# Optimization experiments

Hardware: AMD Instinct MI355X
Metric: run time of the kernel (lower is better)

## Reference

```python
import jax, jax.numpy as jnp
import numpy as np

B, S, H, E, I = 2, 1024, 1024, 8, 512
EPS = 1e-8  # torch F.cosine_similarity eps


def setup_inputs() -> dict:
    key = jax.random.key(0)
    ks = jax.random.split(key, 5)
    return {
        "hidden_states": jax.random.normal(ks[0], (B, S, H), dtype=jnp.float32),
        "expert_embeddings": jax.random.normal(ks[1], (E, H), dtype=jnp.float32),
        # torch init is zeros; -0.03 keeps the zero-selection fallback (which NaNs the
        # original's softmax) from ever triggering while preserving ~half-dense routing
        "gate_threshold": jnp.full((E,), -0.03, dtype=jnp.float32),
        "w_gate": jax.random.normal(ks[2], (E, H, I), dtype=jnp.float32) / np.sqrt(H).astype(np.float32),
        "w_up": jax.random.normal(ks[3], (E, H, I), dtype=jnp.float32) / np.sqrt(H).astype(np.float32),
        "w_down": jax.random.normal(ks[4], (E, I, H), dtype=jnp.float32) / np.sqrt(I).astype(np.float32),
    }


def _forward(hidden_states, expert_embeddings, gate_threshold, w_gate, w_up, w_down):
    b, s, h = hidden_states.shape
    n_experts = expert_embeddings.shape[0]
    x = hidden_states.reshape(-1, h)  # [T, H]

    # cosine-similarity routing scores [T, E]
    xn = x / jnp.maximum(jnp.linalg.norm(x, axis=-1, keepdims=True), EPS)
    en = expert_embeddings / jnp.maximum(jnp.linalg.norm(expert_embeddings, axis=-1, keepdims=True), EPS)
    scores = xn @ en.T

    # SiLUHardThreshold forward: hard 0/1 mask (used only as a boolean downstream,
    # so no gradient flows through it in the module's output path)
    routing_mask = (jax.nn.silu(scores - gate_threshold) > 0).astype(scores.dtype)

    # guarantee at least one expert per token: fall back to top-1 score
    num_sel = routing_mask.sum(axis=-1)  # [T]
    top1 = jnp.argmax(scores, axis=-1)   # [T]
    routing_mask_final = jnp.where((num_sel == 0)[:, None],
                                   jax.nn.one_hot(top1, n_experts, dtype=scores.dtype),
                                   routing_mask)

    # softmax over selected experts (pre-fallback mask, as in the original)
    masked_scores = jnp.where(routing_mask > 0, scores, -jnp.inf)
    routing_weights = jax.nn.softmax(masked_scores.astype(jnp.float32), axis=-1).astype(x.dtype)
    gates = routing_weights * routing_mask_final  # [T, E] combine weights

    # per-expert Qwen3 SwiGLU MLP: down(silu(gate(x)) * up(x)); dense over experts,
    # gated combine is the vectorized equivalent of the gather/MLP/index_add loop
    hmid = jax.nn.silu(jnp.einsum('th,ehi->eti', x, w_gate)) * jnp.einsum('th,ehi->eti', x, w_up)  # [E,T,I]
    out = jnp.einsum('eti,eih,te->th', hmid, w_down, gates)  # [T, H]

    return out.reshape(b, s, h), scores


def reference(hidden_states, expert_embeddings, gate_threshold, w_gate, w_up, w_down):
    # returns (final_hidden_states [B,S,H], router_logits [T,E])
    return _forward(hidden_states, expert_embeddings, gate_threshold, w_gate, w_up, w_down)
```

## Files before the change

### kernel.cpp

```cpp
#include <hip/hip_runtime.h>
#include <hip/hip_bf16.h>
#include <stdint.h>

#define T_TOK 2048
#define H_DIM 1024
#define E_NUM 8
#define I_DIM 512
#define KDOWN (E_NUM * I_DIM)
#define EPSR 1e-8f

typedef short s16x8 __attribute__((ext_vector_type(8)));
typedef float f32x4 __attribute__((ext_vector_type(4)));

static __device__ __forceinline__ uint16_t f2bf(float f) {
    union { float f; uint32_t i; } v; v.f = f;
    uint32_t lsb = (v.i >> 16) & 1u;
    v.i += 0x7fffu + lsb;
    return (uint16_t)(v.i >> 16);
}

static __device__ __forceinline__ void gll16(const void* g, void* l) {
    __builtin_amdgcn_global_load_lds(
        (const __attribute__((address_space(1))) void*)g,
        (__attribute__((address_space(3))) void*)l, 16, 0, 0);
}

__global__ __launch_bounds__(256) void cast_x_kernel(const float* __restrict__ x,
                                                     uint16_t* __restrict__ xb) {
    int i = (blockIdx.x * 256 + threadIdx.x) * 4;
    float4 v = *(const float4*)(x + i);
    ushort4 o;
    o.x = f2bf(v.x); o.y = f2bf(v.y); o.z = f2bf(v.z); o.w = f2bf(v.w);
    *(ushort4*)(xb + i) = o;
}

__global__ __launch_bounds__(256) void transpose_cast_kernel(
    const float* __restrict__ in, uint16_t* __restrict__ out,
    int C, long in_batch, long out_batch, int out_stride) {
    __shared__ float tile[64][68];
    const float* src = in + (long)blockIdx.z * in_batch;
    uint16_t* dst = out + (long)blockIdx.z * out_batch;
    const int r0 = blockIdx.y * 64, c0 = blockIdx.x * 64;
    const int tid = threadIdx.x;
    const int g16 = tid >> 4, l16 = (tid & 15) * 4;
    #pragma unroll
    for (int it = 0; it < 4; ++it) {
        int r = it * 16 + g16;
        *(float4*)&tile[r][l16] = *(const float4*)(src + (long)(r0 + r) * C + c0 + l16);
    }
    __syncthreads();
    #pragma unroll
    for (int it = 0; it < 4; ++it) {
        int oc = it * 16 + g16;
        ushort4 o;
        o.x = f2bf(tile[l16 + 0][oc]);
        o.y = f2bf(tile[l16 + 1][oc]);
        o.z = f2bf(tile[l16 + 2][oc]);
        o.w = f2bf(tile[l16 + 3][oc]);
        *(ushort4*)(dst + (long)(c0 + oc) * out_stride + r0 + l16) = o;
    }
}

__global__ __launch_bounds__(256) void routing_kernel(
    const float* __restrict__ x, const float* __restrict__ emb,
    const float* __restrict__ thr, float* __restrict__ scores_out,
    float* __restrict__ gates) {
    __shared__ float semb[E_NUM * H_DIM];
    __shared__ float senorm[E_NUM];
    const int tid = threadIdx.x;
    const int lane = tid & 63;
    const int wave = tid >> 6;
    for (int i = tid; i < E_NUM * H_DIM; i += 256) semb[i] = emb[i];
    __syncthreads();
    for (int e = wave; e < E_NUM; e += 4) {
        float s = 0.f;
        #pragma unroll
        for (int c = 0; c < 16; ++c) { float v = semb[e * H_DIM + lane + 64 * c]; s += v * v; }
        #pragma unroll
        for (int off = 32; off; off >>= 1) s += __shfl_xor(s, off);
        if (lane == 0) senorm[e] = fmaxf(sqrtf(s), EPSR);
    }
    __syncthreads();
    const int t = blockIdx.x * 4 + wave;
    const float* xt = x + (long)t * H_DIM;
    float nrm = 0.f, dot[E_NUM];
    #pragma unroll
    for (int e = 0; e < E_NUM; ++e) dot[e] = 0.f;
    #pragma unroll
    for (int c = 0; c < 16; ++c) {
        float v = xt[lane + 64 * c];
        nrm += v * v;
        #pragma unroll
        for (int e = 0; e < E_NUM; ++e) dot[e] += v * semb[e * H_DIM + lane + 64 * c];
    }
    #pragma unroll
    for (int off = 32; off; off >>= 1) {
        nrm += __shfl_xor(nrm, off);
        #pragma unroll
        for (int e = 0; e < E_NUM; ++e) dot[e] += __shfl_xor(dot[e], off);
    }
    float xn = fmaxf(sqrtf(nrm), EPSR);
    float sc[E_NUM], sel[E_NUM];
    float msel = -1e30f, mall = -1e30f;
    int nsel = 0, arg = 0;
    #pragma unroll
    for (int e = 0; e < E_NUM; ++e) {
        sc[e] = dot[e] / (xn * senorm[e]);
        float d = sc[e] - thr[e];
        sel[e] = (d > 0.f) ? 1.f : 0.f;
        if (d > 0.f) { nsel++; msel = fmaxf(msel, sc[e]); }
        if (sc[e] > mall) { mall = sc[e]; arg = e; }
    }
    float w[E_NUM], den = 0.f;
    #pragma unroll
    for (int e = 0; e < E_NUM; ++e) { w[e] = (sel[e] > 0.f) ? __expf(sc[e] - msel) : 0.f; den += w[e]; }
    if (lane == 0) {
        #pragma unroll
        for (int e = 0; e < E_NUM; ++e) {
            scores_out[t * E_NUM + e] = sc[e];
            gates[t * E_NUM + e] = (nsel > 0) ? (w[e] / den) : ((e == arg) ? 1.f : 0.f);
        }
    }
}

__global__ __launch_bounds__(256, 4) void moe_gateup_kernel(
    const uint16_t* __restrict__ xb,
    const uint16_t* __restrict__ wgT,
    const uint16_t* __restrict__ wuT,
    const float* __restrict__ gates,
    uint16_t* __restrict__ hmid) {
    const int e  = blockIdx.z;
    const int t0 = blockIdx.x * 128;
    const int i0 = blockIdx.y * 64;
    __shared__ uint16_t sA[128][64];
    __shared__ uint16_t sG[64][64];
    __shared__ uint16_t sU[64][64];
    __shared__ float sGate[128];
    const int tid  = threadIdx.x;
    const int lane = tid & 63;
    const int wave = tid >> 6;
    const int wm = wave >> 1, wn = wave & 1;
    if (tid < 128) sGate[tid] = gates[(t0 + tid) * E_NUM + e];

    const int srowA = wave * 32 + (lane >> 3);
    const int scA   = ((lane & 7) ^ (srowA & 7)) * 8;
    const int srowG = wave * 16 + (lane >> 3);
    const int scG   = ((lane & 7) ^ (srowG & 7)) * 8;
    const uint16_t* ga = xb  + (long)(t0 + srowA) * H_DIM + scA;
    const uint16_t* gg = wgT + ((long)e * I_DIM + i0 + srowG) * H_DIM + scG;
    const uint16_t* gu = wuT + ((long)e * I_DIM + i0 + srowG) * H_DIM + scG;

    f32x4 accg[4][2] = {};
    f32x4 accu[4][2] = {};
    const int q = lane >> 4, r16 = lane & 15;
    const int sw = r16 & 7;

    for (int kb = 0; kb < H_DIM; kb += 64) {
        __syncthreads();
        #pragma unroll
        for (int j = 0; j < 4; ++j)
            gll16(ga + (long)j * 8 * H_DIM + kb, &sA[wave * 32 + j * 8][0]);
        #pragma unroll
        for (int j = 0; j < 2; ++j) {
            gll16(gg + (long)j * 8 * H_DIM + kb, &sG[wave * 16 + j * 8][0]);
            gll16(gu + (long)j * 8 * H_DIM + kb, &sU[wave * 16 + j * 8][0]);
        }
        __syncthreads();
        #pragma unroll
        for (int kk = 0; kk < 2; ++kk) {
            s16x8 af[4], gf[2], uf[2];
            const int pc = ((kk * 4 + q) ^ sw) * 8;
            #pragma unroll
            for (int m = 0; m < 4; ++m)
                af[m] = *(const s16x8*)&sA[wm * 64 + m * 16 + r16][pc];
            #pragma unroll
            for (int n = 0; n < 2; ++n) {
                gf[n] = *(const s16x8*)&sG[wn * 32 + n * 16 + r16][pc];
                uf[n] = *(const s16x8*)&sU[wn * 32 + n * 16 + r16][pc];
            }
            #pragma unroll
            for (int m = 0; m < 4; ++m)
                #pragma unroll
                for (int n = 0; n < 2; ++n) {
                    accg[m][n] = __builtin_amdgcn_mfma_f32_16x16x32_bf16(af[m], gf[n], accg[m][n], 0, 0, 0);
                    accu[m][n] = __builtin_amdgcn_mfma_f32_16x16x32_bf16(af[m], uf[n], accu[m][n], 0, 0, 0);
                }
        }
    }
    #pragma unroll
    for (int m = 0; m < 4; ++m) {
        #pragma unroll
        for (int rr = 0; rr < 4; ++rr) {
            int trow = wm * 64 + m * 16 + q * 4 + rr;
            float gate = sGate[trow];
            long base = (long)(t0 + trow) * KDOWN + e * I_DIM + i0;
            #pragma unroll
            for (int n = 0; n < 2; ++n) {
                float g = accg[m][n][rr], u = accu[m][n][rr];
                float h = gate * (g / (1.f + __expf(-g))) * u;
                hmid[base + wn * 32 + n * 16 + r16] = f2bf(h);
            }
        }
    }
}

__global__ __launch_bounds__(256, 4) void moe_down_kernel(
    const uint16_t* __restrict__ hmid,
    const uint16_t* __restrict__ wdT,
    float* __restrict__ out,
    float* __restrict__ parts) {
    const int t0 = blockIdx.x * 128;
    const int h0 = blockIdx.y * 64;
    const int kz = blockIdx.z;
    const int kst  = kz ? kz * 1344 + 64 : 0;
    const int kend = (kz + 1) * 1344 + 64;
    __shared__ uint16_t sA[128][64];
    __shared__ uint16_t sB[64][64];
    const int tid  = threadIdx.x;
    const int lane = tid & 63;
    const int wave = tid >> 6;
    const int wm = wave >> 1, wn = wave & 1;

    const int srowA = wave * 32 + (lane >> 3);
    const int scA   = ((lane & 7) ^ (srowA & 7)) * 8;
    const int srowB = wave * 16 + (lane >> 3);
    const int scB   = ((lane & 7) ^ (srowB & 7)) * 8;
    const uint16_t* ga = hmid + (long)(t0 + srowA) * KDOWN + scA;
    const uint16_t* gb = wdT  + (long)(h0 + srowB) * KDOWN + scB;

    f32x4 acc[4][2] = {};
    const int q = lane >> 4, r16 = lane & 15;
    const int sw = r16 & 7;

    for (int kb = kst; kb < kend; kb += 64) {
        __syncthreads();
        #pragma unroll
        for (int j = 0; j < 4; ++j)
            gll16(ga + (long)j * 8 * KDOWN + kb, &sA[wave * 32 + j * 8][0]);
        #pragma unroll
        for (int j = 0; j < 2; ++j)
            gll16(gb + (long)j * 8 * KDOWN + kb, &sB[wave * 16 + j * 8][0]);
        __syncthreads();
        #pragma unroll
        for (int kk = 0; kk < 2; ++kk) {
            s16x8 af[4], bf[2];
            const int pc = ((kk * 4 + q) ^ sw) * 8;
            #pragma unroll
            for (int m = 0; m < 4; ++m)
                af[m] = *(const s16x8*)&sA[wm * 64 + m * 16 + r16][pc];
            #pragma unroll
            for (int n = 0; n < 2; ++n)
                bf[n] = *(const s16x8*)&sB[wn * 32 + n * 16 + r16][pc];
            #pragma unroll
            for (int m = 0; m < 4; ++m)
                #pragma unroll
                for (int n = 0; n < 2; ++n)
                    acc[m][n] = __builtin_amdgcn_mfma_f32_16x16x32_bf16(af[m], bf[n], acc[m][n], 0, 0, 0);
        }
    }
    float* dst = (kz == 0) ? out : (parts + (long)(kz - 1) * T_TOK * H_DIM);
    #pragma unroll
    for (int m = 0; m < 4; ++m) {
        #pragma unroll
        for (int rr = 0; rr < 4; ++rr) {
            int t = t0 + wm * 64 + m * 16 + q * 4 + rr;
            #pragma unroll
            for (int n = 0; n < 2; ++n)
                dst[(long)t * H_DIM + h0 + wn * 32 + n * 16 + r16] = acc[m][n][rr];
        }
    }
}

__global__ __launch_bounds__(256) void reduce_kernel(float* __restrict__ out,
                                                     const float* __restrict__ parts) {
    long i = ((long)blockIdx.x * 256 + threadIdx.x) * 4;
    float4 a = *(const float4*)(out + i);
    float4 b = *(const float4*)(parts + i);
    float4 c = *(const float4*)(parts + (long)T_TOK * H_DIM + i);
    a.x += b.x + c.x; a.y += b.y + c.y; a.z += b.z + c.z; a.w += b.w + c.w;
    *(float4*)(out + i) = a;
}

extern "C" void kernel_launch(void* const* d_in, const int* in_sizes, int n_in,
                              void* d_out, int out_size, void* d_ws, size_t ws_size,
                              hipStream_t stream) {
    const float* x    = (const float*)d_in[0];
    const float* emb  = (const float*)d_in[1];
    const float* thr  = (const float*)d_in[2];
    const float* wg   = (const float*)d_in[3];
    const float* wu   = (const float*)d_in[4];
    const float* wd   = (const float*)d_in[5];
    float* out    = (float*)d_out;
    float* scores = out + (size_t)T_TOK * H_DIM;

    uint8_t* ws = (uint8_t*)d_ws;
    uint16_t* xb   = (uint16_t*)(ws);
    uint16_t* wgT  = (uint16_t*)(ws + (size_t)4  * 1048576);
    uint16_t* wuT  = (uint16_t*)(ws + (size_t)12 * 1048576);
    uint16_t* wdT  = (uint16_t*)(ws + (size_t)20 * 1048576);
    uint16_t* hmid = (uint16_t*)(ws + (size_t)28 * 1048576);
    float*    gates = (float*)  (ws + (size_t)44 * 1048576);
    float*    parts = (float*)ws;

    cast_x_kernel<<<(T_TOK * H_DIM) / 1024, 256, 0, stream>>>(x, xb);
    transpose_cast_kernel<<<dim3(I_DIM / 64, H_DIM / 64, E_NUM), 256, 0, stream>>>(
        wg, wgT, I_DIM, (long)H_DIM * I_DIM, (long)I_DIM * H_DIM, H_DIM);
    transpose_cast_kernel<<<dim3(I_DIM / 64, H_DIM / 64, E_NUM), 256, 0, stream>>>(
        wu, wuT, I_DIM, (long)H_DIM * I_DIM, (long)I_DIM * H_DIM, H_DIM);
    transpose_cast_kernel<<<dim3(H_DIM / 64, I_DIM / 64, E_NUM), 256, 0, stream>>>(
        wd, wdT, H_DIM, (long)I_DIM * H_DIM, (long)I_DIM, KDOWN);
    routing_kernel<<<T_TOK / 4, 256, 0, stream>>>(x, emb, thr, scores, gates);
    moe_gateup_kernel<<<dim3(T_TOK / 128, I_DIM / 64, E_NUM), 256, 0, stream>>>(
        xb, wgT, wuT, gates, hmid);
    moe_down_kernel<<<dim3(T_TOK / 128, H_DIM / 64, 3), 256, 0, stream>>>(hmid, wdT, out, parts);
    reduce_kernel<<<(T_TOK * H_DIM) / 1024, 256, 0, stream>>>(out, parts);
}
```

Measured before the change: 190.0 us.

## Fuse prep kernels, double-buffer weights, load activations directly to registers

Merges the three weight transpose-casts into one launch and folds the x-to-bf16 cast into the routing kernel, cutting launches and one pass over x. The gate/up and down GEMMs switch to 256-token tiles where each wave owns 64 full rows and reads its A fragments straight from global memory into registers. Only the weight tiles stay in LDS, now double-buffered so the next tile prefetches during MFMAs. The down GEMM's split-K grows from 3 to 6 slices, with a 5-way partial reduction and the partials buffer moved to its own workspace region. Per-wave accumulator count doubles, which raises register pressure and lowers occupancy, and the uncoalesced direct global A loads are a risk.

```diff
diff --git a/kernel.cpp b/kernel.cpp
--- a/kernel.cpp
+++ b/kernel.cpp
@@ -25,22 +25,26 @@
         (__attribute__((address_space(3))) void*)l, 16, 0, 0);
 }
 
-__global__ __launch_bounds__(256) void cast_x_kernel(const float* __restrict__ x,
-                                                     uint16_t* __restrict__ xb) {
-    int i = (blockIdx.x * 256 + threadIdx.x) * 4;
-    float4 v = *(const float4*)(x + i);
-    ushort4 o;
-    o.x = f2bf(v.x); o.y = f2bf(v.y); o.z = f2bf(v.z); o.w = f2bf(v.w);
-    *(ushort4*)(xb + i) = o;
-}
-
-__global__ __launch_bounds__(256) void transpose_cast_kernel(
-    const float* __restrict__ in, uint16_t* __restrict__ out,
-    int C, long in_batch, long out_batch, int out_stride) {
+__global__ __launch_bounds__(256) void transpose_all_kernel(
+    const float* __restrict__ wg, const float* __restrict__ wu,
+    const float* __restrict__ wd, uint16_t* __restrict__ wgT,
+    uint16_t* __restrict__ wuT, uint16_t* __restrict__ wdT) {
     __shared__ float tile[64][68];
-    const float* src = in + (long)blockIdx.z * in_batch;
-    uint16_t* dst = out + (long)blockIdx.z * out_batch;
-    const int r0 = blockIdx.y * 64, c0 = blockIdx.x * 64;
+    const int z = blockIdx.z;
+    const float* src; uint16_t* dst; int C, out_stride, r0, c0;
+    if (z < 16) {
+        const int e = z & 7;
+        src = (z < 8 ? wg : wu) + (long)e * H_DIM * I_DIM;
+        dst = (z < 8 ? wgT : wuT) + (long)e * I_DIM * H_DIM;
+        C = I_DIM; out_stride = H_DIM;
+        r0 = blockIdx.y * 64; c0 = blockIdx.x * 64;
+    } else {
+        const int e = z - 16;
+        src = wd + (long)e * I_DIM * H_DIM;
+        dst = wdT + (long)e * I_DIM;
+        C = H_DIM; out_stride = KDOWN;
+        r0 = blockIdx.x * 64; c0 = blockIdx.y * 64;
+    }
     const int tid = threadIdx.x;
     const int g16 = tid >> 4, l16 = (tid & 15) * 4;
     #pragma unroll
@@ -64,7 +68,7 @@
 __global__ __launch_bounds__(256) void routing_kernel(
     const float* __restrict__ x, const float* __restrict__ emb,
     const float* __restrict__ thr, float* __restrict__ scores_out,
-    float* __restrict__ gates) {
+    float* __restrict__ gates, uint16_t* __restrict__ xb) {
     __shared__ float semb[E_NUM * H_DIM];
     __shared__ float senorm[E_NUM];
     const int tid = threadIdx.x;
@@ -83,12 +87,14 @@
     __syncthreads();
     const int t = blockIdx.x * 4 + wave;
     const float* xt = x + (long)t * H_DIM;
+    uint16_t* xbt = xb + (long)t * H_DIM;
     float nrm = 0.f, dot[E_NUM];
     #pragma unroll
     for (int e = 0; e < E_NUM; ++e) dot[e] = 0.f;
     #pragma unroll
     for (int c = 0; c < 16; ++c) {
         float v = xt[lane + 64 * c];
+        xbt[lane + 64 * c] = f2bf(v);
         nrm += v * v;
         #pragma unroll
         for (int e = 0; e < E_NUM; ++e) dot[e] += v * semb[e * H_DIM + lane + 64 * c];
@@ -123,150 +129,161 @@
     }
 }
 
-__global__ __launch_bounds__(256, 4) void moe_gateup_kernel(
+__global__ __launch_bounds__(256, 2) void moe_gateup_kernel(
     const uint16_t* __restrict__ xb,
     const uint16_t* __restrict__ wgT,
     const uint16_t* __restrict__ wuT,
     const float* __restrict__ gates,
     uint16_t* __restrict__ hmid) {
     const int e  = blockIdx.z;
-    const int t0 = blockIdx.x * 128;
+    const int t0 = blockIdx.x * 256;
     const int i0 = blockIdx.y * 64;
-    __shared__ uint16_t sA[128][64];
-    __shared__ uint16_t sG[64][64];
-    __shared__ uint16_t sU[64][64];
-    __shared__ float sGate[128];
+    __shared__ uint16_t sG[2][64][64];
+    __shared__ uint16_t sU[2][64][64];
+    __shared__ float sGate[256];
     const int tid  = threadIdx.x;
     const int lane = tid & 63;
     const int wave = tid >> 6;
-    const int wm = wave >> 1, wn = wave & 1;
-    if (tid < 128) sGate[tid] = gates[(t0 + tid) * E_NUM + e];
-
-    const int srowA = wave * 32 + (lane >> 3);
-    const int scA   = ((lane & 7) ^ (srowA & 7)) * 8;
-    const int srowG = wave * 16 + (lane >> 3);
-    const int scG   = ((lane & 7) ^ (srowG & 7)) * 8;
-    const uint16_t* ga = xb  + (long)(t0 + srowA) * H_DIM + scA;
-    const uint16_t* gg = wgT + ((long)e * I_DIM + i0 + srowG) * H_DIM + scG;
-    const uint16_t* gu = wuT + ((long)e * I_DIM + i0 + srowG) * H_DIM + scG;
-
-    f32x4 accg[4][2] = {};
-    f32x4 accu[4][2] = {};
+    sGate[tid] = gates[(t0 + tid) * E_NUM + e];
+
+    const int srow = wave * 16 + (lane >> 3);
+    const int scol = ((lane & 7) ^ (srow & 7)) * 8;
+    const uint16_t* gg = wgT + ((long)e * I_DIM + i0 + srow) * H_DIM + scol;
+    const uint16_t* gu = wuT + ((long)e * I_DIM + i0 + srow) * H_DIM + scol;
+
     const int q = lane >> 4, r16 = lane & 15;
     const int sw = r16 & 7;
-
-    for (int kb = 0; kb < H_DIM; kb += 64) {
-        __syncthreads();
-        #pragma unroll
-        for (int j = 0; j < 4; ++j)
-            gll16(ga + (long)j * 8 * H_DIM + kb, &sA[wave * 32 + j * 8][0]);
-        #pragma unroll
-        for (int j = 0; j < 2; ++j) {
-            gll16(gg + (long)j * 8 * H_DIM + kb, &sG[wave * 16 + j * 8][0]);
-            gll16(gu + (long)j * 8 * H_DIM + kb, &sU[wave * 16 + j * 8][0]);
-        }
-        __syncthreads();
+    const uint16_t* ax = xb + (long)(t0 + wave * 64 + r16) * H_DIM + q * 8;
+
+    f32x4 accg[4][4] = {}, accu[4][4] = {};
+
+    #pragma unroll
+    for (int j = 0; j < 2; ++j) {
+        gll16(gg + (long)j * 8 * H_DIM, &sG[0][wave * 16 + j * 8][0]);
+        gll16(gu + (long)j * 8 * H_DIM, &sU[0][wave * 16 + j * 8][0]);
+    }
+    __syncthreads();
+
+    for (int it = 0; it < 16; ++it) {
+        const int kb = it * 64;
+        const int b = it & 1;
+        s16x8 af[2][4];
+        #pragma unroll
+        for (int kk = 0; kk < 2; ++kk)
+            #pragma unroll
+            for (int m = 0; m < 4; ++m)
+                af[kk][m] = *(const s16x8*)(ax + (long)m * 16 * H_DIM + kb + kk * 32);
+        if (it < 15) {
+            #pragma unroll
+            for (int j = 0; j < 2; ++j) {
+                gll16(gg + (long)j * 8 * H_DIM + kb + 64, &sG[b ^ 1][wave * 16 + j * 8][0]);
+                gll16(gu + (long)j * 8 * H_DIM + kb + 64, &sU[b ^ 1][wave * 16 + j * 8][0]);
+            }
+        }
         #pragma unroll
         for (int kk = 0; kk < 2; ++kk) {
-            s16x8 af[4], gf[2], uf[2];
             const int pc = ((kk * 4 + q) ^ sw) * 8;
-            #pragma unroll
-            for (int m = 0; m < 4; ++m)
-                af[m] = *(const s16x8*)&sA[wm * 64 + m * 16 + r16][pc];
-            #pragma unroll
-            for (int n = 0; n < 2; ++n) {
-                gf[n] = *(const s16x8*)&sG[wn * 32 + n * 16 + r16][pc];
-                uf[n] = *(const s16x8*)&sU[wn * 32 + n * 16 + r16][pc];
+            s16x8 gf[4], uf[4];
+            #pragma unroll
+            for (int n = 0; n < 4; ++n) {
+                gf[n] = *(const s16x8*)&sG[b][n * 16 + r16][pc];
+                uf[n] = *(const s16x8*)&sU[b][n * 16 + r16][pc];
             }
             #pragma unroll
             for (int m = 0; m < 4; ++m)
                 #pragma unroll
-                for (int n = 0; n < 2; ++n) {
-                    accg[m][n] = __builtin_amdgcn_mfma_f32_16x16x32_bf16(af[m], gf[n], accg[m][n], 0, 0, 0);
-                    accu[m][n] = __builtin_amdgcn_mfma_f32_16x16x32_bf16(af[m], uf[n], accu[m][n], 0, 0, 0);
+                for (int n = 0; n < 4; ++n) {
+                    accg[m][n] = __builtin_amdgcn_mfma_f32_16x16x32_bf16(af[kk][m], gf[n], accg[m][n], 0, 0, 0);
+                    accu[m][n] = __builtin_amdgcn_mfma_f32_16x16x32_bf16(af[kk][m], uf[n], accu[m][n], 0, 0, 0);
                 }
         }
+        __syncthreads();
     }
     #pragma unroll
     for (int m = 0; m < 4; ++m) {
         #pragma unroll
         for (int rr = 0; rr < 4; ++rr) {
-            int trow = wm * 64 + m * 16 + q * 4 + rr;
-            float gate = sGate[trow];
-            long base = (long)(t0 + trow) * KDOWN + e * I_DIM + i0;
-            #pragma unroll
-            for (int n = 0; n < 2; ++n) {
+            const int trow = wave * 64 + m * 16 + q * 4 + rr;
+            const float gate = sGate[trow];
+            const long base = (long)(t0 + trow) * KDOWN + e * I_DIM + i0;
+            #pragma unroll
+            for (int n = 0; n < 4; ++n) {
                 float g = accg[m][n][rr], u = accu[m][n][rr];
                 float h = gate * (g / (1.f + __expf(-g))) * u;
-                hmid[base + wn * 32 + n * 16 + r16] = f2bf(h);
+                hmid[base + n * 16 + r16] = f2bf(h);
             }
         }
     }
 }
 
-__global__ __launch_bounds__(256, 4) void moe_down_kernel(
+__global__ __launch_bounds__(256, 3) void moe_down_kernel(
     const uint16_t* __restrict__ hmid,
     const uint16_t* __restrict__ wdT,
     float* __restrict__ out,
     float* __restrict__ parts) {
-    const int t0 = blockIdx.x * 128;
+    const int t0 = blockIdx.x * 256;
     const int h0 = blockIdx.y * 64;
     const int kz = blockIdx.z;
-    const int kst  = kz ? kz * 1344 + 64 : 0;
-    const int kend = (kz + 1) * 1344 + 64;
-    __shared__ uint16_t sA[128][64];
-    __shared__ uint16_t sB[64][64];
+    const int it0 = (kz < 4) ? kz * 11 : 44 + (kz - 4) * 10;
+    const int nit = (kz < 4) ? 11 : 10;
+    __shared__ uint16_t sB[2][64][64];
     const int tid  = threadIdx.x;
     const int lane = tid & 63;
     const int wave = tid >> 6;
-    const int wm = wave >> 1, wn = wave & 1;
-
-    const int srowA = wave * 32 + (lane >> 3);
-    const int scA   = ((lane & 7) ^ (srowA & 7)) * 8;
-    const int srowB = wave * 16 + (lane >> 3);
-    const int scB   = ((lane & 7) ^ (srowB & 7)) * 8;
-    const uint16_t* ga = hmid + (long)(t0 + srowA) * KDOWN + scA;
-    const uint16_t* gb = wdT  + (long)(h0 + srowB) * KDOWN + scB;
-
-    f32x4 acc[4][2] = {};
+
+    const int srow = wave * 16 + (lane >> 3);
+    const int scol = ((lane & 7) ^ (srow & 7)) * 8;
+    const uint16_t* gb = wdT + ((long)h0 + srow) * KDOWN + scol;
+
     const int q = lane >> 4, r16 = lane & 15;
     const int sw = r16 & 7;
-
-    for (int kb = kst; kb < kend; kb += 64) {
-        __syncthreads();
-        #pragma unroll
-        for (int j = 0; j < 4; ++j)
-            gll16(ga + (long)j * 8 * KDOWN + kb, &sA[wave * 32 + j * 8][0]);
-        #pragma unroll
-        for (int j = 0; j < 2; ++j)
-            gll16(gb + (long)j * 8 * KDOWN + kb, &sB[wave * 16 + j * 8][0]);
-        __syncthreads();
+    const uint16_t* ax = hmid + (long)(t0 + wave * 64 + r16) * KDOWN + q * 8;
+
+    f32x4 acc[4][4] = {};
+
+    #pragma unroll
+    for (int j = 0; j < 2; ++j)
+        gll16(gb + (long)it0 * 64 + (long)j * 8 * KDOWN, &sB[0][wave * 16 + j * 8][0]);
+    __syncthreads();
+
+    for (int it = 0; it < nit; ++it) {
+        const int kb = (it0 + it) * 64;
+        const int b = it & 1;
+        s16x8 af[2][4];
+        #pragma unroll
+        for (int kk = 0; kk < 2; ++kk)
+            #pragma unroll
+            for (int m = 0; m < 4; ++m)
+                af[kk][m] = *(const s16x8*)(ax + (long)m * 16 * KDOWN + kb + kk * 32);
+        if (it + 1 < nit) {
+            #pragma unroll
+            for (int j = 0; j < 2; ++j)
+                gll16(gb + (long)(kb + 64) + (long)j * 8 * KDOWN, &sB[b ^ 1][wave * 16 + j * 8][0]);
+        }
         #pragma unroll
         for (int kk = 0; kk < 2; ++kk) {
-            s16x8 af[4], bf[2];
             const int pc = ((kk * 4 + q) ^ sw) * 8;
-            #pragma unroll
-            for (int m = 0; m < 4; ++m)
-                af[m] = *(const s16x8*)&sA[wm * 64 + m * 16 + r16][pc];
-            #pragma unroll
-            for (int n = 0; n < 2; ++n)
-                bf[n] = *(const s16x8*)&sB[wn * 32 + n * 16 + r16][pc];
+            s16x8 bf[4];
+            #pragma unroll
+            for (int n = 0; n < 4; ++n)
+                bf[n] = *(const s16x8*)&sB[b][n * 16 + r16][pc];
             #pragma unroll
             for (int m = 0; m < 4; ++m)
                 #pragma unroll
-                for (int n = 0; n < 2; ++n)
-                    acc[m][n] = __builtin_amdgcn_mfma_f32_16x16x32_bf16(af[m], bf[n], acc[m][n], 0, 0, 0);
-        }
+                for (int n = 0; n < 4; ++n)
+                    acc[m][n] = __builtin_amdgcn_mfma_f32_16x16x32_bf16(af[kk][m], bf[n], acc[m][n], 0, 0, 0);
+        }
+        __syncthreads();
     }
     float* dst = (kz == 0) ? out : (parts + (long)(kz - 1) * T_TOK * H_DIM);
     #pragma unroll
     for (int m = 0; m < 4; ++m) {
         #pragma unroll
         for (int rr = 0; rr < 4; ++rr) {
-            int t = t0 + wm * 64 + m * 16 + q * 4 + rr;
-            #pragma unroll
-            for (int n = 0; n < 2; ++n)
-                dst[(long)t * H_DIM + h0 + wn * 32 + n * 16 + r16] = acc[m][n][rr];
+            const int t = t0 + wave * 64 + m * 16 + q * 4 + rr;
+            #pragma unroll
+            for (int n = 0; n < 4; ++n)
+                dst[(long)t * H_DIM + h0 + n * 16 + r16] = acc[m][n][rr];
         }
     }
 }
@@ -275,9 +292,11 @@
                                                      const float* __restrict__ parts) {
     long i = ((long)blockIdx.x * 256 + threadIdx.x) * 4;
     float4 a = *(const float4*)(out + i);
-    float4 b = *(const float4*)(parts + i);
-    float4 c = *(const float4*)(parts + (long)T_TOK * H_DIM + i);
-    a.x += b.x + c.x; a.y += b.y + c.y; a.z += b.z + c.z; a.w += b.w + c.w;
+    #pragma unroll
+    for (int j = 0; j < 5; ++j) {
+        float4 b = *(const float4*)(parts + (long)j * T_TOK * H_DIM + i);
+        a.x += b.x; a.y += b.y; a.z += b.z; a.w += b.w;
+    }
     *(float4*)(out + i) = a;
 }
 
@@ -300,18 +319,12 @@
     uint16_t* wdT  = (uint16_t*)(ws + (size_t)20 * 1048576);
     uint16_t* hmid = (uint16_t*)(ws + (size_t)28 * 1048576);
     float*    gates = (float*)  (ws + (size_t)44 * 1048576);
-    float*    parts = (float*)ws;
-
-    cast_x_kernel<<<(T_TOK * H_DIM) / 1024, 256, 0, stream>>>(x, xb);
-    transpose_cast_kernel<<<dim3(I_DIM / 64, H_DIM / 64, E_NUM), 256, 0, stream>>>(
-        wg, wgT, I_DIM, (long)H_DIM * I_DIM, (long)I_DIM * H_DIM, H_DIM);
-    transpose_cast_kernel<<<dim3(I_DIM / 64, H_DIM / 64, E_NUM), 256, 0, stream>>>(
-        wu, wuT, I_DIM, (long)H_DIM * I_DIM, (long)I_DIM * H_DIM, H_DIM);
-    transpose_cast_kernel<<<dim3(H_DIM / 64, I_DIM / 64, E_NUM), 256, 0, stream>>>(
-        wd, wdT, H_DIM, (long)I_DIM * H_DIM, (long)I_DIM, KDOWN);
-    routing_kernel<<<T_TOK / 4, 256, 0, stream>>>(x, emb, thr, scores, gates);
-    moe_gateup_kernel<<<dim3(T_TOK / 128, I_DIM / 64, E_NUM), 256, 0, stream>>>(
+    float*    parts = (float*)  (ws + (size_t)48 * 1048576);
+
+    transpose_all_kernel<<<dim3(8, 16, 24), 256, 0, stream>>>(wg, wu, wd, wgT, wuT, wdT);
+    routing_kernel<<<T_TOK / 4, 256, 0, stream>>>(x, emb, thr, scores, gates, xb);
+    moe_gateup_kernel<<<dim3(T_TOK / 256, I_DIM / 64, E_NUM), 256, 0, stream>>>(
         xb, wgT, wuT, gates, hmid);
-    moe_down_kernel<<<dim3(T_TOK / 128, H_DIM / 64, 3), 256, 0, stream>>>(hmid, wdT, out, parts);
+    moe_down_kernel<<<dim3(T_TOK / 256, H_DIM / 64, 6), 256, 0, stream>>>(hmid, wdT, out, parts);
     reduce_kernel<<<(T_TOK * H_DIM) / 1024, 256, 0, stream>>>(out, parts);
 }
```

Result: slower. 210.5 us (+10.8%).
